# Performance work log

Measured on AMD Instinct MI355X. Metric: run time of the kernel, lower is better.

## Reference

```python
import jax, jax.numpy as jnp
import numpy as np

N, E, B = 20000, 320000, 64
IN_DIM, HID, HEADS = 128, 64, 4
NEG_SLOPE = 0.2


def gat_conv(x, edge_index, W, a_src, a_dst, bias, concat):
    """PyG-style GATConv (eval mode, add_self_loops=True)."""
    n = x.shape[0]
    heads, C = a_src.shape
    loops = jnp.arange(n, dtype=edge_index.dtype)
    src = jnp.concatenate([edge_index[0], loops])
    dst = jnp.concatenate([edge_index[1], loops])
    h = (x @ W).reshape(n, heads, C)                      # [N,H,C]
    s_score = jnp.sum(h * a_src[None], axis=-1)           # [N,H]
    d_score = jnp.sum(h * a_dst[None], axis=-1)           # [N,H]
    e = jax.nn.leaky_relu(s_score[src] + d_score[dst], NEG_SLOPE)  # [E',H]
    m = jax.ops.segment_max(e, dst, num_segments=n)       # softmax over incoming edges
    ex = jnp.exp(e - m[dst])
    denom = jax.ops.segment_sum(ex, dst, num_segments=n)
    alpha = ex / (denom[dst] + 1e-16)                     # [E',H]
    out = jax.ops.segment_sum(h[src] * alpha[..., None], dst, num_segments=n)
    out = out.reshape(n, heads * C) if concat else out.mean(axis=1)
    return out + bias


def forward_graph(x, ei, batch, w1, as1, ad1, b1, w2, as2, ad2, b2, w3, as3, ad3, b3):
    x = jax.nn.elu(gat_conv(x, ei, w1, as1, ad1, b1, True))
    x = jax.nn.elu(gat_conv(x, ei, w2, as2, ad2, b2, True))
    x = jax.nn.elu(gat_conv(x, ei, w3, as3, ad3, b3, False))
    s = jax.ops.segment_sum(x, batch, num_segments=B)
    cnt = jax.ops.segment_sum(jnp.ones((x.shape[0],), x.dtype), batch, num_segments=B)
    return s / jnp.maximum(cnt, 1.0)[:, None]


def setup_inputs() -> dict:
    key = jax.random.key(0)
    ks = jax.random.split(key, 24)
    d = {}
    d['x_left'] = jax.random.normal(ks[0], (N, IN_DIM), jnp.float32)
    d['x_right'] = jax.random.normal(ks[1], (N, IN_DIM), jnp.float32)
    d['edge_index_left'] = jax.random.randint(ks[2], (2, E), 0, N, jnp.int32)
    d['edge_index_right'] = jax.random.randint(ks[3], (2, E), 0, N, jnp.int32)
    d['batch_left'] = jnp.sort(jax.random.randint(ks[4], (N,), 0, B, jnp.int32))
    d['batch_right'] = jnp.sort(jax.random.randint(ks[5], (N,), 0, B, jnp.int32))
    sc = 0.05
    d['w1'] = jax.random.normal(ks[6], (IN_DIM, HEADS * HID), jnp.float32) * sc
    d['as1'] = jax.random.normal(ks[7], (HEADS, HID), jnp.float32) * sc
    d['ad1'] = jax.random.normal(ks[8], (HEADS, HID), jnp.float32) * sc
    d['b1'] = jnp.zeros((HEADS * HID,), jnp.float32)
    d['w2'] = jax.random.normal(ks[9], (HEADS * HID, HEADS * HID), jnp.float32) * sc
    d['as2'] = jax.random.normal(ks[10], (HEADS, HID), jnp.float32) * sc
    d['ad2'] = jax.random.normal(ks[11], (HEADS, HID), jnp.float32) * sc
    d['b2'] = jnp.zeros((HEADS * HID,), jnp.float32)
    d['w3'] = jax.random.normal(ks[12], (HEADS * HID, HID), jnp.float32) * sc
    d['as3'] = jax.random.normal(ks[13], (1, HID), jnp.float32) * sc
    d['ad3'] = jax.random.normal(ks[14], (1, HID), jnp.float32) * sc
    d['b3'] = jnp.zeros((HID,), jnp.float32)
    d['fc1_w1'] = jax.random.normal(ks[15], (2 * HID, HID), jnp.float32) * sc
    d['fc1_b1'] = jnp.zeros((HID,), jnp.float32)
    d['fc1_w2'] = jax.random.normal(ks[16], (HID, 2), jnp.float32) * sc
    d['fc1_b2'] = jnp.zeros((2,), jnp.float32)
    d['fc2_w1'] = jax.random.normal(ks[17], (2 * HID, HID), jnp.float32) * sc
    d['fc2_b1'] = jnp.zeros((HID,), jnp.float32)
    d['fc2_w2'] = jax.random.normal(ks[18], (HID, 2), jnp.float32) * sc
    d['fc2_b2'] = jnp.zeros((2,), jnp.float32)
    return d


def reference(x_left, x_right, edge_index_left, edge_index_right, batch_left, batch_right,
              w1, as1, ad1, b1, w2, as2, ad2, b2, w3, as3, ad3, b3,
              fc1_w1, fc1_b1, fc1_w2, fc1_b2, fc2_w1, fc2_b1, fc2_w2, fc2_b2):
    gat = (w1, as1, ad1, b1, w2, as2, ad2, b2, w3, as3, ad3, b3)
    left = forward_graph(x_left, edge_index_left, batch_left, *gat)    # [B,HID]
    right = forward_graph(x_right, edge_index_right, batch_right, *gat)
    emb = jnp.concatenate([left, right], axis=1)                        # [B,2*HID]
    h1 = jax.nn.relu(emb @ fc1_w1 + fc1_b1)
    logits_hc_pd = h1 @ fc1_w2 + fc1_b2
    h2 = jax.nn.relu(emb @ fc2_w1 + fc2_b1)
    logits_pd_dd = h2 @ fc2_w2 + fc2_b2
    return logits_hc_pd, logits_pd_dd
```

## Files before the change

### kernel.cpp

```cpp
#include <hip/hip_runtime.h>
#include <cstdint>
#include <cstddef>

#define NNODES 20000
#define NEDGES 320000
#define NBATCH 64
#define EPRIME (NEDGES + NNODES)
#define SLOTS 64

typedef _Float16 half4 __attribute__((ext_vector_type(4)));
typedef _Float16 half8 __attribute__((ext_vector_type(8)));
typedef float floatx4 __attribute__((ext_vector_type(4)));


__global__ __launch_bounds__(256) void bucket_fill_kernel(const int* __restrict__ eiL,
                                                          const int* __restrict__ eiR,
                                                          int* __restrict__ cnt,
                                                          unsigned short* __restrict__ csr_src) {
    int k = blockIdx.x * 256 + threadIdx.x;
    if (k >= NEDGES) return;
    int side = blockIdx.y;
    const int* ei = side ? eiR : eiL;
    cnt     += side * NNODES;
    csr_src += (size_t)side * NNODES * SLOTS;
    int src = ei[k], dst = ei[NEDGES + k];
    int pos = atomicAdd(&cnt[dst], 1);
    if (pos < SLOTS - 1)
        csr_src[dst * SLOTS + 1 + pos] = (unsigned short)src;
}

__global__ __launch_bounds__(256) void bprep_kernel(const float* __restrict__ w1,
                                                    const float* __restrict__ w2,
                                                    const float* __restrict__ w3,
                                                    _Float16* __restrict__ bf) {
    int id = blockIdx.x * 256 + threadIdx.x;
    const float* B; int ngrp, Nn, base, off;
    if (id < 4096)       { B = w1; ngrp = 16; Nn = 256; base = 0;     off = 0; }
    else if (id < 12288) { B = w2; ngrp = 32; Nn = 256; base = 4096;  off = 32768; }
    else if (id < 14336) { B = w3; ngrp = 32; Nn = 64;  base = 12288; off = 98304; }
    else return;
    int tuple = id - base;
    int c  = tuple & 63;
    int kg = (tuple >> 6) % ngrp;
    int hd = (tuple >> 6) / ngrp;
    half8 hb;
#pragma unroll
    for (int j = 0; j < 8; j++)
        hb[j] = (_Float16)B[(size_t)(kg * 8 + j) * Nn + hd * 64 + c];
    *(half8*)&bf[(size_t)off + (size_t)tuple * 8] = hb;
}

template <typename AT>
__global__ __launch_bounds__(256) void mfma_heads_kernel(const AT* __restrict__ AL,
                                                         const AT* __restrict__ AR,
                                                         const _Float16* __restrict__ Bf,
                                                         _Float16* __restrict__ CL,
                                                         _Float16* __restrict__ CR,
                                                         int M, int K,
                                                         const float* __restrict__ a_src,
                                                         const float* __restrict__ a_dst,
                                                         float* __restrict__ sL,
                                                         float* __restrict__ sR,
                                                         float* __restrict__ dL,
                                                         float* __restrict__ dR) {
    int side = blockIdx.z;
    const AT* A = side ? AR : AL;
    _Float16* C = side ? CR : CL;
    float* s_sc = side ? sR : sL;
    float* d_sc = side ? dR : dL;

    __shared__ __align__(16) char smem[64 * 288 * 2];
    auto Asl = (_Float16 (*)[64][40])smem;

    int t = threadIdx.x;
    int w = t >> 6, lane = t & 63;
    int l4 = lane >> 4, l16 = lane & 15;
    int bm = blockIdx.x * 64;

    int ngrp = K >> 3;
    const _Float16* Bw = Bf + (size_t)w * ngrp * 512;

    int arow = t >> 2;
    int aks = (t & 3) * 8;
    bool arok = (bm + arow) < M;
    const AT* Ap = A + (size_t)(arok ? (bm + arow) : (M - 1)) * K + aks;
    float4 ra0, ra1;
    half8 rh;
    if constexpr (sizeof(AT) == 2) {
        rh = *(const half8*)&Ap[0];
    } else {
        ra0 = *(const float4*)&Ap[0];
        ra1 = *(const float4*)&Ap[4];
    }

    floatx4 acc[4][4] = {};

    int p = 0;
    for (int k0 = 0; k0 < K; k0 += 32, p ^= 1) {
        half8 h0;
        if constexpr (sizeof(AT) == 2) {
            h0 = rh;
        } else {
            h0[0] = (_Float16)ra0.x; h0[1] = (_Float16)ra0.y;
            h0[2] = (_Float16)ra0.z; h0[3] = (_Float16)ra0.w;
            h0[4] = (_Float16)ra1.x; h0[5] = (_Float16)ra1.y;
            h0[6] = (_Float16)ra1.z; h0[7] = (_Float16)ra1.w;
        }
        *(half8*)&Asl[p][arow][aks] = h0;
        int kn = k0 + 32;
        if (kn < K) {
            if constexpr (sizeof(AT) == 2) {
                rh = *(const half8*)&Ap[kn];
            } else {
                ra0 = *(const float4*)&Ap[kn + 0];
                ra1 = *(const float4*)&Ap[kn + 4];
            }
        }
        int kg0 = (k0 >> 3) + l4;
        const _Float16* bp = &Bw[((kg0 << 6) + l16) * 8];
        half8 bf0 = *(const half8*)&bp[0];
        half8 bf1 = *(const half8*)&bp[16 * 8];
        half8 bf2 = *(const half8*)&bp[32 * 8];
        half8 bf3 = *(const half8*)&bp[48 * 8];
        __syncthreads();
        half8 af0 = *(const half8*)&Asl[p][l16][l4 * 8];
        half8 af1 = *(const half8*)&Asl[p][16 + l16][l4 * 8];
        half8 af2 = *(const half8*)&Asl[p][32 + l16][l4 * 8];
        half8 af3 = *(const half8*)&Asl[p][48 + l16][l4 * 8];
        acc[0][0] = __builtin_amdgcn_mfma_f32_16x16x32_f16(af0, bf0, acc[0][0], 0, 0, 0);
        acc[1][0] = __builtin_amdgcn_mfma_f32_16x16x32_f16(af1, bf0, acc[1][0], 0, 0, 0);
        acc[2][0] = __builtin_amdgcn_mfma_f32_16x16x32_f16(af2, bf0, acc[2][0], 0, 0, 0);
        acc[3][0] = __builtin_amdgcn_mfma_f32_16x16x32_f16(af3, bf0, acc[3][0], 0, 0, 0);
        acc[0][1] = __builtin_amdgcn_mfma_f32_16x16x32_f16(af0, bf1, acc[0][1], 0, 0, 0);
        acc[1][1] = __builtin_amdgcn_mfma_f32_16x16x32_f16(af1, bf1, acc[1][1], 0, 0, 0);
        acc[2][1] = __builtin_amdgcn_mfma_f32_16x16x32_f16(af2, bf1, acc[2][1], 0, 0, 0);
        acc[3][1] = __builtin_amdgcn_mfma_f32_16x16x32_f16(af3, bf1, acc[3][1], 0, 0, 0);
        acc[0][2] = __builtin_amdgcn_mfma_f32_16x16x32_f16(af0, bf2, acc[0][2], 0, 0, 0);
        acc[1][2] = __builtin_amdgcn_mfma_f32_16x16x32_f16(af1, bf2, acc[1][2], 0, 0, 0);
        acc[2][2] = __builtin_amdgcn_mfma_f32_16x16x32_f16(af2, bf2, acc[2][2], 0, 0, 0);
        acc[3][2] = __builtin_amdgcn_mfma_f32_16x16x32_f16(af3, bf2, acc[3][2], 0, 0, 0);
        acc[0][3] = __builtin_amdgcn_mfma_f32_16x16x32_f16(af0, bf3, acc[0][3], 0, 0, 0);
        acc[1][3] = __builtin_amdgcn_mfma_f32_16x16x32_f16(af1, bf3, acc[1][3], 0, 0, 0);
        acc[2][3] = __builtin_amdgcn_mfma_f32_16x16x32_f16(af2, bf3, acc[2][3], 0, 0, 0);
        acc[3][3] = __builtin_amdgcn_mfma_f32_16x16x32_f16(af3, bf3, acc[3][3], 0, 0, 0);
    }

    float avv[4], dvv[4];
#pragma unroll
    for (int ni = 0; ni < 4; ni++) {
        avv[ni] = a_src[w * 64 + ni * 16 + l16];
        dvv[ni] = a_dst[w * 64 + ni * 16 + l16];
    }
#pragma unroll
    for (int mi = 0; mi < 4; mi++)
#pragma unroll
    for (int r = 0; r < 4; r++) {
        float ps = acc[mi][0][r] * avv[0] + acc[mi][1][r] * avv[1] +
                   acc[mi][2][r] * avv[2] + acc[mi][3][r] * avv[3];
        float pd = acc[mi][0][r] * dvv[0] + acc[mi][1][r] * dvv[1] +
                   acc[mi][2][r] * dvv[2] + acc[mi][3][r] * dvv[3];
#pragma unroll
        for (int off = 8; off >= 1; off >>= 1) {
            ps += __shfl_xor(ps, off);
            pd += __shfl_xor(pd, off);
        }
        int row = bm + mi * 16 + l4 * 4 + r;
        if (l16 == 0 && row < M) {
            s_sc[row * 4 + w] = ps;
            d_sc[row * 4 + w] = pd;
        }
    }

    __syncthreads();
    auto Cs = (_Float16 (*)[288])smem;
#pragma unroll
    for (int mi = 0; mi < 4; mi++)
#pragma unroll
    for (int ni = 0; ni < 4; ni++)
#pragma unroll
    for (int r = 0; r < 4; r++)
        Cs[mi * 16 + l4 * 4 + r][w * 72 + ni * 16 + l16] = (_Float16)acc[mi][ni][r];
    __syncthreads();
    {
        int row = t >> 2, q = t & 3;
        if (bm + row < M) {
            const half8* sp = (const half8*)&Cs[row][q * 72];
            half8 v0 = sp[0], v1 = sp[1], v2 = sp[2], v3 = sp[3];
            half8 v4 = sp[4], v5 = sp[5], v6 = sp[6], v7 = sp[7];
            half8* dp = (half8*)&C[(size_t)(bm + row) * 256 + q * 64];
            dp[0] = v0; dp[1] = v1; dp[2] = v2; dp[3] = v3;
            dp[4] = v4; dp[5] = v5; dp[6] = v6; dp[7] = v7;
        }
    }
}

__global__ __launch_bounds__(256) void mfma_sides_kernel(const _Float16* __restrict__ AL,
                                                         const _Float16* __restrict__ AR,
                                                         const _Float16* __restrict__ Bf,
                                                         _Float16* __restrict__ CL,
                                                         _Float16* __restrict__ CR,
                                                         int M, int K, int Nn,
                                                         const float* __restrict__ a_src,
                                                         const float* __restrict__ a_dst,
                                                         float* __restrict__ sL,
                                                         float* __restrict__ sR,
                                                         float* __restrict__ dL,
                                                         float* __restrict__ dR,
                                                         int H) {
    int side = blockIdx.z;
    const _Float16* A = side ? AR : AL;
    _Float16* C = side ? CR : CL;
    float* s_sc = side ? sR : sL;
    float* d_sc = side ? dR : dL;

    __shared__ __align__(16) char smemA[2 * 128 * 40 * 2];
    auto Asl = (_Float16 (*)[128][40])smemA;

    int t = threadIdx.x;
    int w = t >> 6, lane = t & 63;
    int l4 = lane >> 4, l16 = lane & 15;
    int bm = blockIdx.x * 128;
    int head = blockIdx.y;
    int bn = head * 64;

    int ngrp = K >> 3;
    const _Float16* Bw = Bf + (size_t)head * ngrp * 512;

    int arow = t >> 1;
    int aks = (t & 1) * 16;
    bool arok = (bm + arow) < M;
    const _Float16* Ap = A + (size_t)(arok ? (bm + arow) : (M - 1)) * K + aks;
    half8 rh0 = *(const half8*)&Ap[0];
    half8 rh1 = *(const half8*)&Ap[8];

    floatx4 acc[2][4] = {};

    int p = 0;
    for (int k0 = 0; k0 < K; k0 += 32, p ^= 1) {
        *(half8*)&Asl[p][arow][aks]     = rh0;
        *(half8*)&Asl[p][arow][aks + 8] = rh1;
        int kn = k0 + 32;
        if (kn < K) {
            rh0 = *(const half8*)&Ap[kn + 0];
            rh1 = *(const half8*)&Ap[kn + 8];
        }
        int kg0 = (k0 >> 3) + l4;
        const _Float16* bp = &Bw[((kg0 << 6) + l16) * 8];
        half8 bf0 = *(const half8*)&bp[0];
        half8 bf1 = *(const half8*)&bp[16 * 8];
        half8 bf2 = *(const half8*)&bp[32 * 8];
        half8 bf3 = *(const half8*)&bp[48 * 8];
        __syncthreads();
        half8 af0 = *(const half8*)&Asl[p][w * 32 + l16][l4 * 8];
        half8 af1 = *(const half8*)&Asl[p][w * 32 + 16 + l16][l4 * 8];
        acc[0][0] = __builtin_amdgcn_mfma_f32_16x16x32_f16(af0, bf0, acc[0][0], 0, 0, 0);
        acc[1][0] = __builtin_amdgcn_mfma_f32_16x16x32_f16(af1, bf0, acc[1][0], 0, 0, 0);
        acc[0][1] = __builtin_amdgcn_mfma_f32_16x16x32_f16(af0, bf1, acc[0][1], 0, 0, 0);
        acc[1][1] = __builtin_amdgcn_mfma_f32_16x16x32_f16(af1, bf1, acc[1][1], 0, 0, 0);
        acc[0][2] = __builtin_amdgcn_mfma_f32_16x16x32_f16(af0, bf2, acc[0][2], 0, 0, 0);
        acc[1][2] = __builtin_amdgcn_mfma_f32_16x16x32_f16(af1, bf2, acc[1][2], 0, 0, 0);
        acc[0][3] = __builtin_amdgcn_mfma_f32_16x16x32_f16(af0, bf3, acc[0][3], 0, 0, 0);
        acc[1][3] = __builtin_amdgcn_mfma_f32_16x16x32_f16(af1, bf3, acc[1][3], 0, 0, 0);
    }

    float avv[4], dvv[4];
#pragma unroll
    for (int ni = 0; ni < 4; ni++) {
        avv[ni] = a_src[head * 64 + ni * 16 + l16];
        dvv[ni] = a_dst[head * 64 + ni * 16 + l16];
    }
#pragma unroll
    for (int mi = 0; mi < 2; mi++)
#pragma unroll
    for (int r = 0; r < 4; r++) {
        float ps = acc[mi][0][r] * avv[0] + acc[mi][1][r] * avv[1] +
                   acc[mi][2][r] * avv[2] + acc[mi][3][r] * avv[3];
        float pd = acc[mi][0][r] * dvv[0] + acc[mi][1][r] * dvv[1] +
                   acc[mi][2][r] * dvv[2] + acc[mi][3][r] * dvv[3];
#pragma unroll
        for (int off = 8; off >= 1; off >>= 1) {
            ps += __shfl_xor(ps, off);
            pd += __shfl_xor(pd, off);
        }
        int row = bm + w * 32 + mi * 16 + l4 * 4 + r;
        if (l16 == 0 && row < M) {
            s_sc[row * H + head] = ps;
            d_sc[row * H + head] = pd;
        }
    }

    __syncthreads();
    auto Cs = (_Float16 (*)[72])smemA;
#pragma unroll
    for (int mi = 0; mi < 2; mi++)
#pragma unroll
    for (int ni = 0; ni < 4; ni++)
#pragma unroll
    for (int r = 0; r < 4; r++)
        Cs[w * 32 + mi * 16 + l4 * 4 + r][ni * 16 + l16] = (_Float16)acc[mi][ni][r];
    __syncthreads();
    {
        int row = t >> 1, hh = t & 1;
        if (bm + row < M) {
            const half8* srcp = (const half8*)&Cs[row][hh * 32];
            half8 v0 = srcp[0], v1 = srcp[1], v2 = srcp[2], v3 = srcp[3];
            half8* dstp = (half8*)&C[(size_t)(bm + row) * Nn + bn + hh * 32];
            dstp[0] = v0; dstp[1] = v1; dstp[2] = v2; dstp[3] = v3;
        }
    }
}

template <int H, int C, typename OT>
__global__ __launch_bounds__(256) void agg_kernel(const _Float16* __restrict__ hL,
                                                  const _Float16* __restrict__ hR,
                                                  const int* __restrict__ cntL,
                                                  const int* __restrict__ cntR,
                                                  const unsigned short* __restrict__ csL,
                                                  const unsigned short* __restrict__ csR,
                                                  const float* __restrict__ sL,
                                                  const float* __restrict__ sR,
                                                  const float* __restrict__ dL,
                                                  const float* __restrict__ dR,
                                                  const float* __restrict__ bias,
                                                  OT* __restrict__ oL,
                                                  OT* __restrict__ oR) {
    constexpr int HC = H * C;
    int side = blockIdx.y;
    const _Float16* hbuf = side ? hR   : hL;
    const int*   cnt     = side ? cntR : cntL;
    const unsigned short* csr_src = side ? csR : csL;
    const float* s_sc    = side ? sR   : sL;
    const float* d_sc    = side ? dR   : dL;
    OT*          out     = side ? oR   : oL;

    __shared__ int   idxb[4][64];
    __shared__ __align__(16) float exb[4][64][H];
    int w = threadIdx.x >> 6, lane = threadIdx.x & 63;
    int n = blockIdx.x * 4 + w;
    if (n >= NNODES) return;
    int r0 = n * SLOTS;
    int deg = min(cnt[n], SLOTS - 1) + 1;

    {
        int sl = 0;
        float exl[H];
#pragma unroll
        for (int h = 0; h < H; h++) exl[h] = 0.f;
        if (lane < deg) {
            sl = (lane == 0) ? n : (int)csr_src[r0 + lane];
#pragma unroll
            for (int h = 0; h < H; h++) {
                float e = s_sc[sl * H + h] + d_sc[n * H + h];
                e = (e >= 0.f) ? e : 0.2f * e;
                exl[h] = expf(e);
            }
        }
        idxb[w][lane] = sl * HC;
        if constexpr (H == 4) {
            *(float4*)&exb[w][lane][0] = make_float4(exl[0], exl[1], exl[2], exl[3]);
        } else {
            exb[w][lane][0] = exl[0];
        }
    }

    float acc[8] = {};
    float den = 0.f;

    if constexpr (H == 4) {
        int hf  = lane >> 5;
        int c32 = lane & 31;
        int hidx = c32 >> 3;
        const _Float16* hb = hbuf + c32 * 8;
        int steps = (deg + 1) >> 1;
        int sb = steps & ~3;
        int s = 0;
        for (; s < sb; s += 4) {
            int e = 2 * s + hf;
            int i0 = idxb[w][e],     i1 = idxb[w][e + 2];
            int i2 = idxb[w][e + 4], i3 = idxb[w][e + 6];
            float w0 = exb[w][e][hidx],     w1 = exb[w][e + 2][hidx];
            float w2 = exb[w][e + 4][hidx], w3 = exb[w][e + 6][hidx];
            half8 v0 = *(const half8*)&hb[i0];
            half8 v1 = *(const half8*)&hb[i1];
            half8 v2 = *(const half8*)&hb[i2];
            half8 v3 = *(const half8*)&hb[i3];
            den += (w0 + w1) + (w2 + w3);
#pragma unroll
            for (int k = 0; k < 8; k++)
                acc[k] += w0 * (float)v0[k] + w1 * (float)v1[k] +
                          w2 * (float)v2[k] + w3 * (float)v3[k];
        }
        for (; s < steps; s++) {
            int e = 2 * s + hf;
            int i0 = idxb[w][e];
            float w0 = exb[w][e][hidx];
            half8 v0 = *(const half8*)&hb[i0];
            den += w0;
#pragma unroll
            for (int k = 0; k < 8; k++) acc[k] += w0 * (float)v0[k];
        }
        den += __shfl_xor(den, 32);
#pragma unroll
        for (int k = 0; k < 8; k++) acc[k] += __shfl_xor(acc[k], 32);
        float inv = 1.0f / (den + 1e-16f);
        int col = c32 * 8 + hf * 4;
        float b0 = bias[col + 0], b1 = bias[col + 1], b2 = bias[col + 2], b3 = bias[col + 3];
        float a0 = hf ? acc[4] : acc[0];
        float a1 = hf ? acc[5] : acc[1];
        float a2 = hf ? acc[6] : acc[2];
        float a3 = hf ? acc[7] : acc[3];
        float r0v = a0 * inv + b0; r0v = (r0v > 0.f) ? r0v : expm1f(r0v);
        float r1v = a1 * inv + b1; r1v = (r1v > 0.f) ? r1v : expm1f(r1v);
        float r2v = a2 * inv + b2; r2v = (r2v > 0.f) ? r2v : expm1f(r2v);
        float r3v = a3 * inv + b3; r3v = (r3v > 0.f) ? r3v : expm1f(r3v);
        if constexpr (sizeof(OT) == 2) {
            half4 v;
            v.x = (_Float16)r0v; v.y = (_Float16)r1v;
            v.z = (_Float16)r2v; v.w = (_Float16)r3v;
            *(half4*)&out[(size_t)n * HC + col] = v;
        } else {
            float4 v = make_float4(r0v, r1v, r2v, r3v);
            *(float4*)&out[(size_t)n * HC + col] = v;
        }
    } else {
        int grp = lane >> 3;
        int c8  = lane & 7;
        const _Float16* hb = hbuf + c8 * 8;
        int steps = (deg + 7) >> 3;
        int sb = steps & ~3;
        int s = 0;
        for (; s < sb; s += 4) {
            int e = s * 8 + grp;
            int i0 = idxb[w][e],      i1 = idxb[w][e + 8];
            int i2 = idxb[w][e + 16], i3 = idxb[w][e + 24];
            float w0 = exb[w][e][0],      w1 = exb[w][e + 8][0];
            float w2 = exb[w][e + 16][0], w3 = exb[w][e + 24][0];
            half8 v0 = *(const half8*)&hb[i0];
            half8 v1 = *(const half8*)&hb[i1];
            half8 v2 = *(const half8*)&hb[i2];
            half8 v3 = *(const half8*)&hb[i3];
            den += (w0 + w1) + (w2 + w3);
#pragma unroll
            for (int k = 0; k < 8; k++)
                acc[k] += w0 * (float)v0[k] + w1 * (float)v1[k] +
                          w2 * (float)v2[k] + w3 * (float)v3[k];
        }
        for (; s < steps; s++) {
            int e = s * 8 + grp;
            int i0 = idxb[w][e];
            float w0 = exb[w][e][0];
            half8 v0 = *(const half8*)&hb[i0];
            den += w0;
#pragma unroll
            for (int k = 0; k < 8; k++) acc[k] += w0 * (float)v0[k];
        }
#pragma unroll
        for (int off = 8; off <= 32; off <<= 1) {
            den += __shfl_xor(den, off);
#pragma unroll
            for (int k = 0; k < 8; k++) acc[k] += __shfl_xor(acc[k], off);
        }
        if (lane < 16) {
            float inv = 1.0f / (den + 1e-16f);
            int sub = lane >> 3;
            int col = (lane & 7) * 8 + sub * 4;
            float a0 = sub ? acc[4] : acc[0];
            float a1 = sub ? acc[5] : acc[1];
            float a2 = sub ? acc[6] : acc[2];
            float a3 = sub ? acc[7] : acc[3];
            float r0v = a0 * inv + bias[col + 0]; r0v = (r0v > 0.f) ? r0v : expm1f(r0v);
            float r1v = a1 * inv + bias[col + 1]; r1v = (r1v > 0.f) ? r1v : expm1f(r1v);
            float r2v = a2 * inv + bias[col + 2]; r2v = (r2v > 0.f) ? r2v : expm1f(r2v);
            float r3v = a3 * inv + bias[col + 3]; r3v = (r3v > 0.f) ? r3v : expm1f(r3v);
            if constexpr (sizeof(OT) == 2) {
                half4 v;
                v.x = (_Float16)r0v; v.y = (_Float16)r1v;
                v.z = (_Float16)r2v; v.w = (_Float16)r3v;
                *(half4*)&out[(size_t)n * HC + col] = v;
            } else {
                float4 v = make_float4(r0v, r1v, r2v, r3v);
                *(float4*)&out[(size_t)n * HC + col] = v;
            }
        }
    }
}

__global__ __launch_bounds__(256) void pool_kernel(const float* __restrict__ xL,
                                                   const float* __restrict__ xR,
                                                   const int* __restrict__ baL,
                                                   const int* __restrict__ baR,
                                                   float* __restrict__ pL,
                                                   float* __restrict__ pR,
                                                   float* __restrict__ cL,
                                                   float* __restrict__ cR) {
    int side = blockIdx.y;
    const float* x     = side ? xR  : xL;
    const int*   batch = side ? baR : baL;
    float* pooled = side ? pR : pL;
    float* cntb   = side ? cR : cL;

    int b = blockIdx.x;
    int lo = 0, hi = NNODES;
    while (lo < hi) { int mid = (lo + hi) >> 1; if (batch[mid] < b) lo = mid + 1; else hi = mid; }
    int start = lo;
    hi = NNODES;
    while (lo < hi) { int mid = (lo + hi) >> 1; if (batch[mid] < b + 1) lo = mid + 1; else hi = mid; }
    int end = lo;

    int t = threadIdx.x;
    int c = t & 63, g = t >> 6;
    float s = 0.f;
    for (int n = start + g; n < end; n += 4) s += x[n * 64 + c];
    __shared__ float buf[4][64];
    buf[g][c] = s;
    __syncthreads();
    if (t < 64) {
        pooled[b * 64 + t] = buf[0][t] + buf[1][t] + buf[2][t] + buf[3][t];
        if (t == 0) cntb[b] = (float)(end - start);
    }
}

__global__ __launch_bounds__(256) void head_kernel(const float* __restrict__ pL,
                                                   const float* __restrict__ cL,
                                                   const float* __restrict__ pR,
                                                   const float* __restrict__ cR,
                                                   const float* __restrict__ w1a,
                                                   const float* __restrict__ b1a,
                                                   const float* __restrict__ w2a,
                                                   const float* __restrict__ b2a,
                                                   const float* __restrict__ w1b,
                                                   const float* __restrict__ b1b,
                                                   const float* __restrict__ w2b,
                                                   const float* __restrict__ b2b,
                                                   float* __restrict__ out) {
    int b = blockIdx.x;
    int t = threadIdx.x;
    __shared__ float emb[128];
    __shared__ float ph[4][64];
    __shared__ float h1[64];
    if (t < 64)        emb[t] = pL[b * 64 + t] / fmaxf(cL[b], 1.0f);
    else if (t < 128)  emb[t] = pR[b * 64 + (t - 64)] / fmaxf(cR[b], 1.0f);
    __syncthreads();
    int c = t & 63, g = t >> 6;
    {
        float p = 0.f;
#pragma unroll
        for (int k = 0; k < 32; k++) p += emb[g * 32 + k] * w1a[(g * 32 + k) * 64 + c];
        ph[g][c] = p;
        __syncthreads();
        if (t < 64) h1[t] = fmaxf(ph[0][t] + ph[1][t] + ph[2][t] + ph[3][t] + b1a[t], 0.f);
        __syncthreads();
        if (t < 128) {
            int o = t >> 6, lane = t & 63;
            float q = h1[lane] * w2a[lane * 2 + o];
#pragma unroll
            for (int off = 32; off >= 1; off >>= 1) q += __shfl_xor(q, off);
            if (lane == 0) out[b * 2 + o] = q + b2a[o];
        }
        __syncthreads();
    }
    {
        float p = 0.f;
#pragma unroll
        for (int k = 0; k < 32; k++) p += emb[g * 32 + k] * w1b[(g * 32 + k) * 64 + c];
        ph[g][c] = p;
        __syncthreads();
        if (t < 64) h1[t] = fmaxf(ph[0][t] + ph[1][t] + ph[2][t] + ph[3][t] + b1b[t], 0.f);
        __syncthreads();
        if (t < 128) {
            int o = t >> 6, lane = t & 63;
            float q = h1[lane] * w2b[lane * 2 + o];
#pragma unroll
            for (int off = 32; off >= 1; off >>= 1) q += __shfl_xor(q, off);
            if (lane == 0) out[128 + b * 2 + o] = q + b2b[o];
        }
    }
}

extern "C" void kernel_launch(void* const* d_in, const int* in_sizes, int n_in,
                              void* d_out, int out_size, void* d_ws, size_t ws_size,
                              hipStream_t stream) {
    const float* x_left   = (const float*)d_in[0];
    const float* x_right  = (const float*)d_in[1];
    const int*   ei_left  = (const int*)d_in[2];
    const int*   ei_right = (const int*)d_in[3];
    const int*   ba_left  = (const int*)d_in[4];
    const int*   ba_right = (const int*)d_in[5];
    const float* w1  = (const float*)d_in[6];
    const float* as1 = (const float*)d_in[7];
    const float* ad1 = (const float*)d_in[8];
    const float* b1  = (const float*)d_in[9];
    const float* w2  = (const float*)d_in[10];
    const float* as2 = (const float*)d_in[11];
    const float* ad2 = (const float*)d_in[12];
    const float* b2  = (const float*)d_in[13];
    const float* w3  = (const float*)d_in[14];
    const float* as3 = (const float*)d_in[15];
    const float* ad3 = (const float*)d_in[16];
    const float* b3  = (const float*)d_in[17];
    const float* f1w1 = (const float*)d_in[18];
    const float* f1b1 = (const float*)d_in[19];
    const float* f1w2 = (const float*)d_in[20];
    const float* f1b2 = (const float*)d_in[21];
    const float* f2w1 = (const float*)d_in[22];
    const float* f2b1 = (const float*)d_in[23];
    const float* f2w2 = (const float*)d_in[24];
    const float* f2b2 = (const float*)d_in[25];

    const size_t NEED = (size_t)95 * 1024 * 1024;
    int ns = (ws_size >= NEED) ? 2 : 1;

    char* w = (char*)d_ws;
    auto carve = [&](size_t bytes) {
        void* p = (void*)w;
        w += (bytes + 255) & ~(size_t)255;
        return p;
    };
    const size_t HSTR = (size_t)NNODES * 256;
    _Float16* hbf  = (_Float16*)carve((size_t)ns * HSTR * 2);
    _Float16* obf  = (_Float16*)carve((size_t)ns * HSTR * 2);
    float* o3bf    = (float*)carve((size_t)ns * NNODES * 64 * 4);
    float* s_sc    = (float*)carve((size_t)ns * NNODES * 4 * 4);
    float* d_sc    = (float*)carve((size_t)ns * NNODES * 4 * 4);
    int*   cnt     = (int*)carve((size_t)ns * NNODES * 4);
    unsigned short* csr = (unsigned short*)carve((size_t)ns * NNODES * SLOTS * 2);
    float* pooled  = (float*)carve(2 * 64 * 64 * 4);
    float* cntb    = (float*)carve(2 * 64 * 4);
    _Float16* bfw  = (_Float16*)carve(114688 * 2);

    _Float16* bf1 = bfw;
    _Float16* bf2 = bfw + 32768;
    _Float16* bf3 = bfw + 98304;

    const int egrid  = (NEDGES + 255) / 256;
    const int ngrid  = (NNODES + 3) / 4;
    const int mgrid64  = (NNODES + 63) / 64;
    const int mgrid128 = (NNODES + 127) / 128;

    if (ns == 2) {
        _Float16* h_L = hbf;          _Float16* h_R = hbf + HSTR;
        _Float16* o_L = obf;          _Float16* o_R = obf + HSTR;
        float* o3_L = o3bf;           float* o3_R = o3bf + (size_t)NNODES * 64;
        float* sL = s_sc;             float* sR = s_sc + NNODES * 4;
        float* dL = d_sc;             float* dR = d_sc + NNODES * 4;
        int* cnL = cnt;               int* cnR = cnt + NNODES;
        unsigned short* csL = csr;    unsigned short* csR = csr + (size_t)NNODES * SLOTS;

        hipMemsetAsync(cnt, 0, (size_t)2 * NNODES * 4, stream);
        bprep_kernel<<<56, 256, 0, stream>>>(w1, w2, w3, bfw);
        bucket_fill_kernel<<<dim3(egrid, 2), 256, 0, stream>>>(ei_left, ei_right, cnt, csr);

        mfma_heads_kernel<float><<<dim3(mgrid64, 1, 2), 256, 0, stream>>>(
            x_left, x_right, bf1, h_L, h_R, NNODES, 128, as1, ad1, sL, sR, dL, dR);
        agg_kernel<4, 64, _Float16><<<dim3(ngrid, 2), 256, 0, stream>>>(
            h_L, h_R, cnL, cnR, csL, csR, sL, sR, dL, dR, b1, o_L, o_R);
        mfma_heads_kernel<_Float16><<<dim3(mgrid64, 1, 2), 256, 0, stream>>>(
            o_L, o_R, bf2, h_L, h_R, NNODES, 256, as2, ad2, sL, sR, dL, dR);
        agg_kernel<4, 64, _Float16><<<dim3(ngrid, 2), 256, 0, stream>>>(
            h_L, h_R, cnL, cnR, csL, csR, sL, sR, dL, dR, b2, o_L, o_R);
        mfma_sides_kernel<<<dim3(mgrid128, 1, 2), 256, 0, stream>>>(
            o_L, o_R, bf3, h_L, h_R, NNODES, 256, 64, as3, ad3, sL, sR, dL, dR, 1);
        agg_kernel<1, 64, float><<<dim3(ngrid, 2), 256, 0, stream>>>(
            h_L, h_R, cnL, cnR, csL, csR, sL, sR, dL, dR, b3, o3_L, o3_R);

        pool_kernel<<<dim3(NBATCH, 2), 256, 0, stream>>>(
            o3_L, o3_R, ba_left, ba_right, pooled, pooled + 4096, cntb, cntb + 64);
        head_kernel<<<NBATCH, 256, 0, stream>>>(pooled, cntb, pooled + 4096, cntb + 64,
                                                f1w1, f1b1, f1w2, f1b2,
                                                f2w1, f2b1, f2w2, f2b2,
                                                (float*)d_out);
    } else {
        bprep_kernel<<<56, 256, 0, stream>>>(w1, w2, w3, bfw);
        for (int side = 0; side < 2; side++) {
            const float* x_in  = side ? x_right  : x_left;
            const int*   ei    = side ? ei_right : ei_left;
            const int*   batch = side ? ba_right : ba_left;
            float* pside = pooled + side * 4096;
            float* cside = cntb + side * 64;

            hipMemsetAsync(cnt, 0, (size_t)NNODES * 4, stream);
            bucket_fill_kernel<<<dim3(egrid, 1), 256, 0, stream>>>(ei, ei, cnt, csr);

            mfma_heads_kernel<float><<<dim3(mgrid64, 1, 1), 256, 0, stream>>>(
                x_in, x_in, bf1, hbf, hbf, NNODES, 128, as1, ad1, s_sc, s_sc, d_sc, d_sc);
            agg_kernel<4, 64, _Float16><<<dim3(ngrid, 1), 256, 0, stream>>>(
                hbf, hbf, cnt, cnt, csr, csr, s_sc, s_sc, d_sc, d_sc, b1, obf, obf);

            mfma_heads_kernel<_Float16><<<dim3(mgrid64, 1, 1), 256, 0, stream>>>(
                obf, obf, bf2, hbf, hbf, NNODES, 256, as2, ad2, s_sc, s_sc, d_sc, d_sc);
            agg_kernel<4, 64, _Float16><<<dim3(ngrid, 1), 256, 0, stream>>>(
                hbf, hbf, cnt, cnt, csr, csr, s_sc, s_sc, d_sc, d_sc, b2, obf, obf);

            mfma_sides_kernel<<<dim3(mgrid128, 1, 1), 256, 0, stream>>>(
                obf, obf, bf3, hbf, hbf, NNODES, 256, 64, as3, ad3, s_sc, s_sc, d_sc, d_sc, 1);
            agg_kernel<1, 64, float><<<dim3(ngrid, 1), 256, 0, stream>>>(
                hbf, hbf, cnt, cnt, csr, csr, s_sc, s_sc, d_sc, d_sc, b3, o3bf, o3bf);

            pool_kernel<<<dim3(NBATCH, 1), 256, 0, stream>>>(
                o3bf, o3bf, batch, batch, pside, pside, cside, cside);
        }
        head_kernel<<<NBATCH, 256, 0, stream>>>(pooled, cntb, pooled + 4096, cntb + 64,
                                                f1w1, f1b1, f1w2, f1b2,
                                                f2w1, f2b1, f2w2, f2b2,
                                                (float*)d_out);
    }
}
```

Baseline: 349.0 us.

## Fuse edge bucket fill into layer-1 GEMM and fold pooling into last aggregation

The edge bucketing work now runs as extra blocks in the same launch as the first-layer MFMA GEMM, so the two independent phases share one grid and one launch. The last-layer aggregation now accumulates ELU outputs straight into per-graph pooled sums with atomics, replacing the separate pool kernel and the fp32 intermediate buffer. This saves two launches and one round trip of the layer-3 activations through memory. In exchange it adds float atomic contention on the 64 graph slots, order-dependent summation, and a memset of the pooled buffer.

```diff
diff --git a/kernel.cpp b/kernel.cpp
--- a/kernel.cpp
+++ b/kernel.cpp
@@ -5,29 +5,14 @@
 #define NNODES 20000
 #define NEDGES 320000
 #define NBATCH 64
-#define EPRIME (NEDGES + NNODES)
 #define SLOTS 64
+#define MG64  ((NNODES + 63) / 64)
+#define FILLB ((NEDGES + 255) / 256)
 
 typedef _Float16 half4 __attribute__((ext_vector_type(4)));
 typedef _Float16 half8 __attribute__((ext_vector_type(8)));
 typedef float floatx4 __attribute__((ext_vector_type(4)));
 
-
-__global__ __launch_bounds__(256) void bucket_fill_kernel(const int* __restrict__ eiL,
-                                                          const int* __restrict__ eiR,
-                                                          int* __restrict__ cnt,
-                                                          unsigned short* __restrict__ csr_src) {
-    int k = blockIdx.x * 256 + threadIdx.x;
-    if (k >= NEDGES) return;
-    int side = blockIdx.y;
-    const int* ei = side ? eiR : eiL;
-    cnt     += side * NNODES;
-    csr_src += (size_t)side * NNODES * SLOTS;
-    int src = ei[k], dst = ei[NEDGES + k];
-    int pos = atomicAdd(&cnt[dst], 1);
-    if (pos < SLOTS - 1)
-        csr_src[dst * SLOTS + 1 + pos] = (unsigned short)src;
-}
 
 __global__ __launch_bounds__(256) void bprep_kernel(const float* __restrict__ w1,
                                                     const float* __restrict__ w2,
@@ -51,31 +36,21 @@
 }
 
 template <typename AT>
-__global__ __launch_bounds__(256) void mfma_heads_kernel(const AT* __restrict__ AL,
-                                                         const AT* __restrict__ AR,
-                                                         const _Float16* __restrict__ Bf,
-                                                         _Float16* __restrict__ CL,
-                                                         _Float16* __restrict__ CR,
-                                                         int M, int K,
-                                                         const float* __restrict__ a_src,
-                                                         const float* __restrict__ a_dst,
-                                                         float* __restrict__ sL,
-                                                         float* __restrict__ sR,
-                                                         float* __restrict__ dL,
-                                                         float* __restrict__ dR) {
-    int side = blockIdx.z;
-    const AT* A = side ? AR : AL;
-    _Float16* C = side ? CR : CL;
-    float* s_sc = side ? sR : sL;
-    float* d_sc = side ? dR : dL;
-
-    __shared__ __align__(16) char smem[64 * 288 * 2];
+__device__ __forceinline__ void mfma_heads_body(char* smem,
+                                                const AT* __restrict__ A,
+                                                const _Float16* __restrict__ Bf,
+                                                _Float16* __restrict__ C,
+                                                int M, int K,
+                                                const float* __restrict__ a_src,
+                                                const float* __restrict__ a_dst,
+                                                float* __restrict__ s_sc,
+                                                float* __restrict__ d_sc,
+                                                int bm) {
     auto Asl = (_Float16 (*)[64][40])smem;
 
     int t = threadIdx.x;
     int w = t >> 6, lane = t & 63;
     int l4 = lane >> 4, l16 = lane & 15;
-    int bm = blockIdx.x * 64;
 
     int ngrp = K >> 3;
     const _Float16* Bw = Bf + (size_t)w * ngrp * 512;
@@ -194,6 +169,61 @@
     }
 }
 
+template <typename AT>
+__global__ __launch_bounds__(256) void mfma_heads_kernel(const AT* __restrict__ AL,
+                                                         const AT* __restrict__ AR,
+                                                         const _Float16* __restrict__ Bf,
+                                                         _Float16* __restrict__ CL,
+                                                         _Float16* __restrict__ CR,
+                                                         int M, int K,
+                                                         const float* __restrict__ a_src,
+                                                         const float* __restrict__ a_dst,
+                                                         float* __restrict__ sL,
+                                                         float* __restrict__ sR,
+                                                         float* __restrict__ dL,
+                                                         float* __restrict__ dR) {
+    __shared__ __align__(16) char smem[64 * 288 * 2];
+    int side = blockIdx.z;
+    mfma_heads_body<AT>(smem, side ? AR : AL, Bf, side ? CR : CL, M, K,
+                        a_src, a_dst, side ? sR : sL, side ? dR : dL,
+                        blockIdx.x * 64);
+}
+
+__global__ __launch_bounds__(256) void l1_fill_kernel(const float* __restrict__ xL,
+                                                      const float* __restrict__ xR,
+                                                      const _Float16* __restrict__ Bf,
+                                                      _Float16* __restrict__ CL,
+                                                      _Float16* __restrict__ CR,
+                                                      int M, int K,
+                                                      const float* __restrict__ a_src,
+                                                      const float* __restrict__ a_dst,
+                                                      float* __restrict__ sL,
+                                                      float* __restrict__ sR,
+                                                      float* __restrict__ dL,
+                                                      float* __restrict__ dR,
+                                                      const int* __restrict__ eiL,
+                                                      const int* __restrict__ eiR,
+                                                      int* __restrict__ cnt,
+                                                      unsigned short* __restrict__ csr_src) {
+    __shared__ __align__(16) char smem[64 * 288 * 2];
+    int side = blockIdx.z;
+    if (blockIdx.x < MG64) {
+        mfma_heads_body<float>(smem, side ? xR : xL, Bf, side ? CR : CL, M, K,
+                               a_src, a_dst, side ? sR : sL, side ? dR : dL,
+                               blockIdx.x * 64);
+    } else {
+        int k = (blockIdx.x - MG64) * 256 + threadIdx.x;
+        if (k >= NEDGES) return;
+        const int* ei = side ? eiR : eiL;
+        int* c = cnt + side * NNODES;
+        unsigned short* cs = csr_src + (size_t)side * NNODES * SLOTS;
+        int src = ei[k], dst = ei[NEDGES + k];
+        int pos = atomicAdd(&c[dst], 1);
+        if (pos < SLOTS - 1)
+            cs[dst * SLOTS + 1 + pos] = (unsigned short)src;
+    }
+}
+
 __global__ __launch_bounds__(256) void mfma_sides_kernel(const _Float16* __restrict__ AL,
                                                          const _Float16* __restrict__ AR,
                                                          const _Float16* __restrict__ Bf,
@@ -310,31 +340,30 @@
     }
 }
 
-template <int H, int C, typename OT>
-__global__ __launch_bounds__(256) void agg_kernel(const _Float16* __restrict__ hL,
-                                                  const _Float16* __restrict__ hR,
-                                                  const int* __restrict__ cntL,
-                                                  const int* __restrict__ cntR,
-                                                  const unsigned short* __restrict__ csL,
-                                                  const unsigned short* __restrict__ csR,
-                                                  const float* __restrict__ sL,
-                                                  const float* __restrict__ sR,
-                                                  const float* __restrict__ dL,
-                                                  const float* __restrict__ dR,
-                                                  const float* __restrict__ bias,
-                                                  OT* __restrict__ oL,
-                                                  OT* __restrict__ oR) {
-    constexpr int HC = H * C;
+__global__ __launch_bounds__(256) void agg4_kernel(const _Float16* __restrict__ hL,
+                                                   const _Float16* __restrict__ hR,
+                                                   const int* __restrict__ cntL,
+                                                   const int* __restrict__ cntR,
+                                                   const unsigned short* __restrict__ csL,
+                                                   const unsigned short* __restrict__ csR,
+                                                   const float* __restrict__ sL,
+                                                   const float* __restrict__ sR,
+                                                   const float* __restrict__ dL,
+                                                   const float* __restrict__ dR,
+                                                   const float* __restrict__ bias,
+                                                   _Float16* __restrict__ oL,
+                                                   _Float16* __restrict__ oR) {
+    constexpr int HC = 256;
     int side = blockIdx.y;
     const _Float16* hbuf = side ? hR   : hL;
     const int*   cnt     = side ? cntR : cntL;
     const unsigned short* csr_src = side ? csR : csL;
     const float* s_sc    = side ? sR   : sL;
     const float* d_sc    = side ? dR   : dL;
-    OT*          out     = side ? oR   : oL;
+    _Float16*    out     = side ? oR   : oL;
 
     __shared__ int   idxb[4][64];
-    __shared__ __align__(16) float exb[4][64][H];
+    __shared__ __align__(16) float exb[4][64][4];
     int w = threadIdx.x >> 6, lane = threadIdx.x & 63;
     int n = blockIdx.x * 4 + w;
     if (n >= NNODES) return;
@@ -343,180 +372,183 @@
 
     {
         int sl = 0;
-        float exl[H];
-#pragma unroll
-        for (int h = 0; h < H; h++) exl[h] = 0.f;
+        float exl[4] = {0.f, 0.f, 0.f, 0.f};
         if (lane < deg) {
             sl = (lane == 0) ? n : (int)csr_src[r0 + lane];
 #pragma unroll
-            for (int h = 0; h < H; h++) {
-                float e = s_sc[sl * H + h] + d_sc[n * H + h];
+            for (int h = 0; h < 4; h++) {
+                float e = s_sc[sl * 4 + h] + d_sc[n * 4 + h];
                 e = (e >= 0.f) ? e : 0.2f * e;
                 exl[h] = expf(e);
             }
         }
         idxb[w][lane] = sl * HC;
-        if constexpr (H == 4) {
-            *(float4*)&exb[w][lane][0] = make_float4(exl[0], exl[1], exl[2], exl[3]);
-        } else {
-            exb[w][lane][0] = exl[0];
-        }
+        *(float4*)&exb[w][lane][0] = make_float4(exl[0], exl[1], exl[2], exl[3]);
     }
 
     float acc[8] = {};
     float den = 0.f;
 
-    if constexpr (H == 4) {
-        int hf  = lane >> 5;
-        int c32 = lane & 31;
-        int hidx = c32 >> 3;
-        const _Float16* hb = hbuf + c32 * 8;
-        int steps = (deg + 1) >> 1;
-        int sb = steps & ~3;
-        int s = 0;
-        for (; s < sb; s += 4) {
-            int e = 2 * s + hf;
-            int i0 = idxb[w][e],     i1 = idxb[w][e + 2];
-            int i2 = idxb[w][e + 4], i3 = idxb[w][e + 6];
-            float w0 = exb[w][e][hidx],     w1 = exb[w][e + 2][hidx];
-            float w2 = exb[w][e + 4][hidx], w3 = exb[w][e + 6][hidx];
-            half8 v0 = *(const half8*)&hb[i0];
-            half8 v1 = *(const half8*)&hb[i1];
-            half8 v2 = *(const half8*)&hb[i2];
-            half8 v3 = *(const half8*)&hb[i3];
-            den += (w0 + w1) + (w2 + w3);
-#pragma unroll
-            for (int k = 0; k < 8; k++)
-                acc[k] += w0 * (float)v0[k] + w1 * (float)v1[k] +
-                          w2 * (float)v2[k] + w3 * (float)v3[k];
-        }
-        for (; s < steps; s++) {
-            int e = 2 * s + hf;
-            int i0 = idxb[w][e];
-            float w0 = exb[w][e][hidx];
-            half8 v0 = *(const half8*)&hb[i0];
-            den += w0;
-#pragma unroll
-            for (int k = 0; k < 8; k++) acc[k] += w0 * (float)v0[k];
-        }
-        den += __shfl_xor(den, 32);
-#pragma unroll
-        for (int k = 0; k < 8; k++) acc[k] += __shfl_xor(acc[k], 32);
+    int hf  = lane >> 5;
+    int c32 = lane & 31;
+    int hidx = c32 >> 3;
+    const _Float16* hb = hbuf + c32 * 8;
+    int steps = (deg + 1) >> 1;
+    int sb = steps & ~3;
+    int s = 0;
+    for (; s < sb; s += 4) {
+        int e = 2 * s + hf;
+        int i0 = idxb[w][e],     i1 = idxb[w][e + 2];
+        int i2 = idxb[w][e + 4], i3 = idxb[w][e + 6];
+        float w0 = exb[w][e][hidx],     w1 = exb[w][e + 2][hidx];
+        float w2 = exb[w][e + 4][hidx], w3 = exb[w][e + 6][hidx];
+        half8 v0 = *(const half8*)&hb[i0];
+        half8 v1 = *(const half8*)&hb[i1];
+        half8 v2 = *(const half8*)&hb[i2];
+        half8 v3 = *(const half8*)&hb[i3];
+        den += (w0 + w1) + (w2 + w3);
+#pragma unroll
+        for (int k = 0; k < 8; k++)
+            acc[k] += w0 * (float)v0[k] + w1 * (float)v1[k] +
+                      w2 * (float)v2[k] + w3 * (float)v3[k];
+    }
+    for (; s < steps; s++) {
+        int e = 2 * s + hf;
+        int i0 = idxb[w][e];
+        float w0 = exb[w][e][hidx];
+        half8 v0 = *(const half8*)&hb[i0];
+        den += w0;
+#pragma unroll
+        for (int k = 0; k < 8; k++) acc[k] += w0 * (float)v0[k];
+    }
+    den += __shfl_xor(den, 32);
+#pragma unroll
+    for (int k = 0; k < 8; k++) acc[k] += __shfl_xor(acc[k], 32);
+    float inv = 1.0f / (den + 1e-16f);
+    int col = c32 * 8 + hf * 4;
+    float b0 = bias[col + 0], b1 = bias[col + 1], b2 = bias[col + 2], b3 = bias[col + 3];
+    float a0 = hf ? acc[4] : acc[0];
+    float a1 = hf ? acc[5] : acc[1];
+    float a2 = hf ? acc[6] : acc[2];
+    float a3 = hf ? acc[7] : acc[3];
+    float r0v = a0 * inv + b0; r0v = (r0v > 0.f) ? r0v : expm1f(r0v);
+    float r1v = a1 * inv + b1; r1v = (r1v > 0.f) ? r1v : expm1f(r1v);
+    float r2v = a2 * inv + b2; r2v = (r2v > 0.f) ? r2v : expm1f(r2v);
+    float r3v = a3 * inv + b3; r3v = (r3v > 0.f) ? r3v : expm1f(r3v);
+    half4 v;
+    v.x = (_Float16)r0v; v.y = (_Float16)r1v;
+    v.z = (_Float16)r2v; v.w = (_Float16)r3v;
+    *(half4*)&out[(size_t)n * HC + col] = v;
+}
+
+__global__ __launch_bounds__(256) void agg_pool_kernel(const _Float16* __restrict__ hL,
+                                                       const _Float16* __restrict__ hR,
+                                                       const int* __restrict__ cntL,
+                                                       const int* __restrict__ cntR,
+                                                       const unsigned short* __restrict__ csL,
+                                                       const unsigned short* __restrict__ csR,
+                                                       const float* __restrict__ sL,
+                                                       const float* __restrict__ sR,
+                                                       const float* __restrict__ dL,
+                                                       const float* __restrict__ dR,
+                                                       const float* __restrict__ bias,
+                                                       const int* __restrict__ baL,
+                                                       const int* __restrict__ baR,
+                                                       float* __restrict__ pL,
+                                                       float* __restrict__ pR,
+                                                       float* __restrict__ cbL,
+                                                       float* __restrict__ cbR) {
+    constexpr int HC = 64;
+    int side = blockIdx.y;
+    const _Float16* hbuf = side ? hR   : hL;
+    const int*   cnt     = side ? cntR : cntL;
+    const unsigned short* csr_src = side ? csR : csL;
+    const float* s_sc    = side ? sR   : sL;
+    const float* d_sc    = side ? dR   : dL;
+    const int*   batch   = side ? baR  : baL;
+    float*       pooled  = side ? pR   : pL;
+    float*       cb      = side ? cbR  : cbL;
+
+    __shared__ int   idxb[4][64];
+    __shared__ __align__(16) float exb[4][64][1];
+    int w = threadIdx.x >> 6, lane = threadIdx.x & 63;
+    int n = blockIdx.x * 4 + w;
+    if (n >= NNODES) return;
+    int r0 = n * SLOTS;
+    int deg = min(cnt[n], SLOTS - 1) + 1;
+
+    {
+        int sl = 0;
+        float exl = 0.f;
+        if (lane < deg) {
+            sl = (lane == 0) ? n : (int)csr_src[r0 + lane];
+            float e = s_sc[sl] + d_sc[n];
+            e = (e >= 0.f) ? e : 0.2f * e;
+            exl = expf(e);
+        }
+        idxb[w][lane] = sl * HC;
+        exb[w][lane][0] = exl;
+    }
+
+    float acc[8] = {};
+    float den = 0.f;
+
+    int grp = lane >> 3;
+    int c8  = lane & 7;
+    const _Float16* hb = hbuf + c8 * 8;
+    int steps = (deg + 7) >> 3;
+    int sb = steps & ~3;
+    int s = 0;
+    for (; s < sb; s += 4) {
+        int e = s * 8 + grp;
+        int i0 = idxb[w][e],      i1 = idxb[w][e + 8];
+        int i2 = idxb[w][e + 16], i3 = idxb[w][e + 24];
+        float w0 = exb[w][e][0],      w1 = exb[w][e + 8][0];
+        float w2 = exb[w][e + 16][0], w3 = exb[w][e + 24][0];
+        half8 v0 = *(const half8*)&hb[i0];
+        half8 v1 = *(const half8*)&hb[i1];
+        half8 v2 = *(const half8*)&hb[i2];
+        half8 v3 = *(const half8*)&hb[i3];
+        den += (w0 + w1) + (w2 + w3);
+#pragma unroll
+        for (int k = 0; k < 8; k++)
+            acc[k] += w0 * (float)v0[k] + w1 * (float)v1[k] +
+                      w2 * (float)v2[k] + w3 * (float)v3[k];
+    }
+    for (; s < steps; s++) {
+        int e = s * 8 + grp;
+        int i0 = idxb[w][e];
+        float w0 = exb[w][e][0];
+        half8 v0 = *(const half8*)&hb[i0];
+        den += w0;
+#pragma unroll
+        for (int k = 0; k < 8; k++) acc[k] += w0 * (float)v0[k];
+    }
+#pragma unroll
+    for (int off = 8; off <= 32; off <<= 1) {
+        den += __shfl_xor(den, off);
+#pragma unroll
+        for (int k = 0; k < 8; k++) acc[k] += __shfl_xor(acc[k], off);
+    }
+    int bn = batch[n];
+    if (lane < 16) {
         float inv = 1.0f / (den + 1e-16f);
-        int col = c32 * 8 + hf * 4;
-        float b0 = bias[col + 0], b1 = bias[col + 1], b2 = bias[col + 2], b3 = bias[col + 3];
-        float a0 = hf ? acc[4] : acc[0];
-        float a1 = hf ? acc[5] : acc[1];
-        float a2 = hf ? acc[6] : acc[2];
-        float a3 = hf ? acc[7] : acc[3];
-        float r0v = a0 * inv + b0; r0v = (r0v > 0.f) ? r0v : expm1f(r0v);
-        float r1v = a1 * inv + b1; r1v = (r1v > 0.f) ? r1v : expm1f(r1v);
-        float r2v = a2 * inv + b2; r2v = (r2v > 0.f) ? r2v : expm1f(r2v);
-        float r3v = a3 * inv + b3; r3v = (r3v > 0.f) ? r3v : expm1f(r3v);
-        if constexpr (sizeof(OT) == 2) {
-            half4 v;
-            v.x = (_Float16)r0v; v.y = (_Float16)r1v;
-            v.z = (_Float16)r2v; v.w = (_Float16)r3v;
-            *(half4*)&out[(size_t)n * HC + col] = v;
-        } else {
-            float4 v = make_float4(r0v, r1v, r2v, r3v);
-            *(float4*)&out[(size_t)n * HC + col] = v;
-        }
-    } else {
-        int grp = lane >> 3;
-        int c8  = lane & 7;
-        const _Float16* hb = hbuf + c8 * 8;
-        int steps = (deg + 7) >> 3;
-        int sb = steps & ~3;
-        int s = 0;
-        for (; s < sb; s += 4) {
-            int e = s * 8 + grp;
-            int i0 = idxb[w][e],      i1 = idxb[w][e + 8];
-            int i2 = idxb[w][e + 16], i3 = idxb[w][e + 24];
-            float w0 = exb[w][e][0],      w1 = exb[w][e + 8][0];
-            float w2 = exb[w][e + 16][0], w3 = exb[w][e + 24][0];
-            half8 v0 = *(const half8*)&hb[i0];
-            half8 v1 = *(const half8*)&hb[i1];
-            half8 v2 = *(const half8*)&hb[i2];
-            half8 v3 = *(const half8*)&hb[i3];
-            den += (w0 + w1) + (w2 + w3);
-#pragma unroll
-            for (int k = 0; k < 8; k++)
-                acc[k] += w0 * (float)v0[k] + w1 * (float)v1[k] +
-                          w2 * (float)v2[k] + w3 * (float)v3[k];
-        }
-        for (; s < steps; s++) {
-            int e = s * 8 + grp;
-            int i0 = idxb[w][e];
-            float w0 = exb[w][e][0];
-            half8 v0 = *(const half8*)&hb[i0];
-            den += w0;
-#pragma unroll
-            for (int k = 0; k < 8; k++) acc[k] += w0 * (float)v0[k];
-        }
-#pragma unroll
-        for (int off = 8; off <= 32; off <<= 1) {
-            den += __shfl_xor(den, off);
-#pragma unroll
-            for (int k = 0; k < 8; k++) acc[k] += __shfl_xor(acc[k], off);
-        }
-        if (lane < 16) {
-            float inv = 1.0f / (den + 1e-16f);
-            int sub = lane >> 3;
-            int col = (lane & 7) * 8 + sub * 4;
-            float a0 = sub ? acc[4] : acc[0];
-            float a1 = sub ? acc[5] : acc[1];
-            float a2 = sub ? acc[6] : acc[2];
-            float a3 = sub ? acc[7] : acc[3];
-            float r0v = a0 * inv + bias[col + 0]; r0v = (r0v > 0.f) ? r0v : expm1f(r0v);
-            float r1v = a1 * inv + bias[col + 1]; r1v = (r1v > 0.f) ? r1v : expm1f(r1v);
-            float r2v = a2 * inv + bias[col + 2]; r2v = (r2v > 0.f) ? r2v : expm1f(r2v);
-            float r3v = a3 * inv + bias[col + 3]; r3v = (r3v > 0.f) ? r3v : expm1f(r3v);
-            if constexpr (sizeof(OT) == 2) {
-                half4 v;
-                v.x = (_Float16)r0v; v.y = (_Float16)r1v;
-                v.z = (_Float16)r2v; v.w = (_Float16)r3v;
-                *(half4*)&out[(size_t)n * HC + col] = v;
-            } else {
-                float4 v = make_float4(r0v, r1v, r2v, r3v);
-                *(float4*)&out[(size_t)n * HC + col] = v;
-            }
-        }
-    }
-}
-
-__global__ __launch_bounds__(256) void pool_kernel(const float* __restrict__ xL,
-                                                   const float* __restrict__ xR,
-                                                   const int* __restrict__ baL,
-                                                   const int* __restrict__ baR,
-                                                   float* __restrict__ pL,
-                                                   float* __restrict__ pR,
-                                                   float* __restrict__ cL,
-                                                   float* __restrict__ cR) {
-    int side = blockIdx.y;
-    const float* x     = side ? xR  : xL;
-    const int*   batch = side ? baR : baL;
-    float* pooled = side ? pR : pL;
-    float* cntb   = side ? cR : cL;
-
-    int b = blockIdx.x;
-    int lo = 0, hi = NNODES;
-    while (lo < hi) { int mid = (lo + hi) >> 1; if (batch[mid] < b) lo = mid + 1; else hi = mid; }
-    int start = lo;
-    hi = NNODES;
-    while (lo < hi) { int mid = (lo + hi) >> 1; if (batch[mid] < b + 1) lo = mid + 1; else hi = mid; }
-    int end = lo;
-
-    int t = threadIdx.x;
-    int c = t & 63, g = t >> 6;
-    float s = 0.f;
-    for (int n = start + g; n < end; n += 4) s += x[n * 64 + c];
-    __shared__ float buf[4][64];
-    buf[g][c] = s;
-    __syncthreads();
-    if (t < 64) {
-        pooled[b * 64 + t] = buf[0][t] + buf[1][t] + buf[2][t] + buf[3][t];
-        if (t == 0) cntb[b] = (float)(end - start);
+        int sub = lane >> 3;
+        int col = (lane & 7) * 8 + sub * 4;
+        float a0 = sub ? acc[4] : acc[0];
+        float a1 = sub ? acc[5] : acc[1];
+        float a2 = sub ? acc[6] : acc[2];
+        float a3 = sub ? acc[7] : acc[3];
+        float r0v = a0 * inv + bias[col + 0]; r0v = (r0v > 0.f) ? r0v : expm1f(r0v);
+        float r1v = a1 * inv + bias[col + 1]; r1v = (r1v > 0.f) ? r1v : expm1f(r1v);
+        float r2v = a2 * inv + bias[col + 2]; r2v = (r2v > 0.f) ? r2v : expm1f(r2v);
+        float r3v = a3 * inv + bias[col + 3]; r3v = (r3v > 0.f) ? r3v : expm1f(r3v);
+        float* pp = &pooled[bn * 64 + col];
+        atomicAdd(&pp[0], r0v);
+        atomicAdd(&pp[1], r1v);
+        atomicAdd(&pp[2], r2v);
+        atomicAdd(&pp[3], r3v);
+        if (lane == 0) atomicAdd(&cb[bn], 1.0f);
     }
 }
 
@@ -619,7 +651,6 @@
     const size_t HSTR = (size_t)NNODES * 256;
     _Float16* hbf  = (_Float16*)carve((size_t)ns * HSTR * 2);
     _Float16* obf  = (_Float16*)carve((size_t)ns * HSTR * 2);
-    float* o3bf    = (float*)carve((size_t)ns * NNODES * 64 * 4);
     float* s_sc    = (float*)carve((size_t)ns * NNODES * 4 * 4);
     float* d_sc    = (float*)carve((size_t)ns * NNODES * 4 * 4);
     int*   cnt     = (int*)carve((size_t)ns * NNODES * 4);
@@ -632,44 +663,42 @@
     _Float16* bf2 = bfw + 32768;
     _Float16* bf3 = bfw + 98304;
 
-    const int egrid  = (NEDGES + 255) / 256;
-    const int ngrid  = (NNODES + 3) / 4;
-    const int mgrid64  = (NNODES + 63) / 64;
+    const int ngrid    = (NNODES + 3) / 4;
     const int mgrid128 = (NNODES + 127) / 128;
 
     if (ns == 2) {
         _Float16* h_L = hbf;          _Float16* h_R = hbf + HSTR;
         _Float16* o_L = obf;          _Float16* o_R = obf + HSTR;
-        float* o3_L = o3bf;           float* o3_R = o3bf + (size_t)NNODES * 64;
         float* sL = s_sc;             float* sR = s_sc + NNODES * 4;
         float* dL = d_sc;             float* dR = d_sc + NNODES * 4;
         int* cnL = cnt;               int* cnR = cnt + NNODES;
         unsigned short* csL = csr;    unsigned short* csR = csr + (size_t)NNODES * SLOTS;
 
         hipMemsetAsync(cnt, 0, (size_t)2 * NNODES * 4, stream);
+        hipMemsetAsync(pooled, 0, 2 * 64 * 64 * 4 + 2 * 64 * 4, stream);
         bprep_kernel<<<56, 256, 0, stream>>>(w1, w2, w3, bfw);
-        bucket_fill_kernel<<<dim3(egrid, 2), 256, 0, stream>>>(ei_left, ei_right, cnt, csr);
-
-        mfma_heads_kernel<float><<<dim3(mgrid64, 1, 2), 256, 0, stream>>>(
-            x_left, x_right, bf1, h_L, h_R, NNODES, 128, as1, ad1, sL, sR, dL, dR);
-        agg_kernel<4, 64, _Float16><<<dim3(ngrid, 2), 256, 0, stream>>>(
+
+        l1_fill_kernel<<<dim3(MG64 + FILLB, 1, 2), 256, 0, stream>>>(
+            x_left, x_right, bf1, h_L, h_R, NNODES, 128, as1, ad1, sL, sR, dL, dR,
+            ei_left, ei_right, cnt, csr);
+        agg4_kernel<<<dim3(ngrid, 2), 256, 0, stream>>>(
             h_L, h_R, cnL, cnR, csL, csR, sL, sR, dL, dR, b1, o_L, o_R);
-        mfma_heads_kernel<_Float16><<<dim3(mgrid64, 1, 2), 256, 0, stream>>>(
+        mfma_heads_kernel<_Float16><<<dim3(MG64, 1, 2), 256, 0, stream>>>(
             o_L, o_R, bf2, h_L, h_R, NNODES, 256, as2, ad2, sL, sR, dL, dR);
-        agg_kernel<4, 64, _Float16><<<dim3(ngrid, 2), 256, 0, stream>>>(
+        agg4_kernel<<<dim3(ngrid, 2), 256, 0, stream>>>(
             h_L, h_R, cnL, cnR, csL, csR, sL, sR, dL, dR, b2, o_L, o_R);
         mfma_sides_kernel<<<dim3(mgrid128, 1, 2), 256, 0, stream>>>(
             o_L, o_R, bf3, h_L, h_R, NNODES, 256, 64, as3, ad3, sL, sR, dL, dR, 1);
-        agg_kernel<1, 64, float><<<dim3(ngrid, 2), 256, 0, stream>>>(
-            h_L, h_R, cnL, cnR, csL, csR, sL, sR, dL, dR, b3, o3_L, o3_R);
-
-        pool_kernel<<<dim3(NBATCH, 2), 256, 0, stream>>>(
-            o3_L, o3_R, ba_left, ba_right, pooled, pooled + 4096, cntb, cntb + 64);
+        agg_pool_kernel<<<dim3(ngrid, 2), 256, 0, stream>>>(
+            h_L, h_R, cnL, cnR, csL, csR, sL, sR, dL, dR, b3,
+            ba_left, ba_right, pooled, pooled + 4096, cntb, cntb + 64);
+
         head_kernel<<<NBATCH, 256, 0, stream>>>(pooled, cntb, pooled + 4096, cntb + 64,
                                                 f1w1, f1b1, f1w2, f1b2,
                                                 f2w1, f2b1, f2w2, f2b2,
                                                 (float*)d_out);
     } else {
+        hipMemsetAsync(pooled, 0, 2 * 64 * 64 * 4 + 2 * 64 * 4, stream);
         bprep_kernel<<<56, 256, 0, stream>>>(w1, w2, w3, bfw);
         for (int side = 0; side < 2; side++) {
             const float* x_in  = side ? x_right  : x_left;
@@ -679,25 +708,22 @@
             float* cside = cntb + side * 64;
 
             hipMemsetAsync(cnt, 0, (size_t)NNODES * 4, stream);
-            bucket_fill_kernel<<<dim3(egrid, 1), 256, 0, stream>>>(ei, ei, cnt, csr);
-
-            mfma_heads_kernel<float><<<dim3(mgrid64, 1, 1), 256, 0, stream>>>(
-                x_in, x_in, bf1, hbf, hbf, NNODES, 128, as1, ad1, s_sc, s_sc, d_sc, d_sc);
-            agg_kernel<4, 64, _Float16><<<dim3(ngrid, 1), 256, 0, stream>>>(
+            l1_fill_kernel<<<dim3(MG64 + FILLB, 1, 1), 256, 0, stream>>>(
+                x_in, x_in, bf1, hbf, hbf, NNODES, 128, as1, ad1,
+                s_sc, s_sc, d_sc, d_sc, ei, ei, cnt, csr);
+            agg4_kernel<<<dim3(ngrid, 1), 256, 0, stream>>>(
                 hbf, hbf, cnt, cnt, csr, csr, s_sc, s_sc, d_sc, d_sc, b1, obf, obf);
 
-            mfma_heads_kernel<_Float16><<<dim3(mgrid64, 1, 1), 256, 0, stream>>>(
+            mfma_heads_kernel<_Float16><<<dim3(MG64, 1, 1), 256, 0, stream>>>(
                 obf, obf, bf2, hbf, hbf, NNODES, 256, as2, ad2, s_sc, s_sc, d_sc, d_sc);
-            agg_kernel<4, 64, _Float16><<<dim3(ngrid, 1), 256, 0, stream>>>(
+            agg4_kernel<<<dim3(ngrid, 1), 256, 0, stream>>>(
                 hbf, hbf, cnt, cnt, csr, csr, s_sc, s_sc, d_sc, d_sc, b2, obf, obf);
 
             mfma_sides_kernel<<<dim3(mgrid128, 1, 1), 256, 0, stream>>>(
                 obf, obf, bf3, hbf, hbf, NNODES, 256, 64, as3, ad3, s_sc, s_sc, d_sc, d_sc, 1);
-            agg_kernel<1, 64, float><<<dim3(ngrid, 1), 256, 0, stream>>>(
-                hbf, hbf, cnt, cnt, csr, csr, s_sc, s_sc, d_sc, d_sc, b3, o3bf, o3bf);
-
-            pool_kernel<<<dim3(NBATCH, 1), 256, 0, stream>>>(
-                o3bf, o3bf, batch, batch, pside, pside, cside, cside);
+            agg_pool_kernel<<<dim3(ngrid, 1), 256, 0, stream>>>(
+                hbf, hbf, cnt, cnt, csr, csr, s_sc, s_sc, d_sc, d_sc, b3,
+                batch, batch, pside, pside, cside, cside);
         }
         head_kernel<<<NBATCH, 256, 0, stream>>>(pooled, cntb, pooled + 4096, cntb + 64,
                                                 f1w1, f1b1, f1w2, f1b2,
```

Result: slower. 505.8 us (+44.9%).
